# Performance work log

Hardware: AMD Instinct MI355X
Metric: run time of the kernel (lower is better)

Reference implementation:

```python
import jax, jax.numpy as jnp
import numpy as np

D, K, CIN, CD, COUT = 3, 16, 128, 32, 256
C = CIN + CD                  # 160 = C_in + C_delta after concat
DM = -(-COUT // C)            # depth_multiplier = ceil(C_out / C) = 2
N, I = 4, 2048                # batch, points per cloud; M = N*I = 8192


def _bn(x, g, b, eps=1e-5):
    # BatchNorm1d in training mode: biased batch statistics over dim 0
    mu = x.mean(0)
    v = x.var(0)
    return (x - mu) * jax.lax.rsqrt(v + eps) * g + b


def _knn(p, k):
    # knn_graph over ALL M points (wrapper passes no batch vector), loop=True
    d2 = jnp.sum(p * p, axis=1)
    dist = d2[:, None] + d2[None, :] - 2.0 * (p @ p.T)   # [M,M]
    _, idx = jax.lax.top_k(-dist, k)                     # [M,K], self first
    return idx


def _gconv(t, w, b, M):
    # grouped Conv1d(K, K*K, kernel=K, groups=K): t [M,K,K], w [K(cin), K(out/grp), K(tap)]
    return jnp.einsum('mcl,col->mco', t, w).reshape(M, K * K) + b


def _xconv(xf, pf, idx, w1a, b1a, g1a, be1a, w1b, b1b, g1b, be1b,
           w2, b2, g2a, be2a, wc2a, bc2a, g2b, be2b, wc2b, bc2b, g2c, be2c,
           wcd, bcd, wl, bl):
    M = pf.shape[0]
    rel = pf[idx] - pf[:, None, :]                       # [M,K,D] relative neighbor coords
    # mlp1: lift relative coords to C_delta features
    h = rel.reshape(M * K, D)
    h = _bn(jax.nn.elu(h @ w1a + b1a), g1a, be1a)
    h = _bn(jax.nn.elu(h @ w1b + b1b), g1b, be1b)
    x_star = jnp.concatenate([h.reshape(M, K, CD), xf[idx]], axis=-1)  # [M,K,C]
    x_star = x_star.transpose(0, 2, 1)                   # [M,C,K]
    # mlp2: learn KxK X-transformation from the K*D relative coords
    t = _bn(jax.nn.elu(rel.reshape(M, K * D) @ w2 + b2), g2a, be2a).reshape(M, K, K)
    t = _bn(jax.nn.elu(_gconv(t, wc2a, bc2a, M)), g2b, be2b).reshape(M, K, K)
    t = _bn(_gconv(t, wc2b, bc2b, M), g2c, be2c).reshape(M, K, K)
    xt = jnp.einsum('mck,mkj->mcj', x_star, t)           # [M,C,K] batched matmul
    # depthwise Conv1d(C, C*DM, K, groups=C) collapses K, then final Linear
    y = jnp.einsum('mcl,col->mco', xt, wcd).reshape(M, C * DM) + bcd
    return y @ wl + bl                                   # [M,COUT]


def setup_inputs() -> dict:
    key = jax.random.key(0)
    ks = jax.random.split(key, 16)
    r = lambda k, s: jax.random.normal(k, s, jnp.float32) * 0.1
    return dict(
        x=jax.random.normal(ks[0], (N, I, CIN), jnp.float32),
        pos=jax.random.normal(ks[1], (N, I, D), jnp.float32),
        w1a=r(ks[2], (D, CD)), b1a=r(ks[3], (CD,)), g1a=jnp.ones((CD,)), be1a=jnp.zeros((CD,)),
        w1b=r(ks[4], (CD, CD)), b1b=r(ks[5], (CD,)), g1b=jnp.ones((CD,)), be1b=jnp.zeros((CD,)),
        w2=r(ks[6], (D * K, K * K)), b2=r(ks[7], (K * K,)), g2a=jnp.ones((K * K,)), be2a=jnp.zeros((K * K,)),
        wc2a=r(ks[8], (K, K, K)), bc2a=r(ks[9], (K * K,)), g2b=jnp.ones((K * K,)), be2b=jnp.zeros((K * K,)),
        wc2b=r(ks[10], (K, K, K)), bc2b=r(ks[11], (K * K,)), g2c=jnp.ones((K * K,)), be2c=jnp.zeros((K * K,)),
        wcd=r(ks[12], (C, DM, K)), bcd=r(ks[13], (C * DM,)),
        wl=r(ks[14], (C * DM, COUT)), bl=r(ks[15], (COUT,)),
    )


def reference(x, pos, w1a, b1a, g1a, be1a, w1b, b1b, g1b, be1b,
              w2, b2, g2a, be2a, wc2a, bc2a, g2b, be2b, wc2b, bc2b, g2c, be2c,
              wcd, bcd, wl, bl):
    pf = pos.reshape(N * I, D)
    xf = x.reshape(N * I, CIN)
    idx = _knn(pf, K)
    out = _xconv(xf, pf, idx, w1a, b1a, g1a, be1a, w1b, b1b, g1b, be1b,
                 w2, b2, g2a, be2a, wc2a, bc2a, g2b, be2b, wc2b, bc2b, g2c, be2c,
                 wcd, bcd, wl, bl)
    return out.reshape(N, I, COUT)
```

## Files before the change

### kernel.cpp

```cpp
#include <hip/hip_runtime.h>
#include <math.h>

#define M_PTS 8192
#define MK    131072

typedef __attribute__((ext_vector_type(8))) short bf16x8;
typedef __attribute__((ext_vector_type(4))) float f32x4;
typedef __fp16 half2v __attribute__((ext_vector_type(2)));
union H2U { half2v h; unsigned u; };

__device__ __forceinline__ float elu(float v){ return v > 0.f ? v : __expf(v)-1.0f; }

__device__ __forceinline__ unsigned cvt_pk_bf16(float lo, float hi){
  unsigned r;
  asm("v_cvt_pk_bf16_f32 %0, %1, %2" : "=v"(r) : "v"(lo), "v"(hi));
  return r;
}
__device__ __forceinline__ unsigned short f2bf(float v){
  unsigned u = __float_as_uint(v);
  return (unsigned short)((u + 0x7FFFu + ((u>>16)&1u)) >> 16);
}
__device__ __forceinline__ unsigned pk_min_u16(unsigned a, unsigned b){
  unsigned r; asm("v_pk_min_u16 %0, %1, %2" : "=v"(r) : "v"(a), "v"(b)); return r;
}
__device__ __forceinline__ unsigned pk_max_u16(unsigned a, unsigned b){
  unsigned r; asm("v_pk_max_u16 %0, %1, %2" : "=v"(r) : "v"(a), "v"(b)); return r;
}

__device__ __forceinline__ unsigned distkey(float4 c, float qx, float qy, float qz, float d2q){
  #pragma clang fp contract(off)
  float dot  = __builtin_fmaf(c.z, qz, __builtin_fmaf(c.y, qy, __builtin_fmaf(c.x, qx, 0.0f)));
  float A    = d2q + c.w;
  float B    = 2.0f * dot;
  float dist = A - B;
  unsigned u = __float_as_uint(dist);
  return u ^ ((unsigned)((int)u >> 31) | 0x80000000u);
}

__global__ __launch_bounds__(512) void knn_kernel(const float* __restrict__ pos,
                                                  int* __restrict__ nidx,
                                                  float* __restrict__ st,
                                                  float4* __restrict__ pos4){
  __shared__ float4 cand[1024];
  __shared__ unsigned long long hits[8][64];
  int tid  = threadIdx.x;
  int lane = tid & 63;
  int wv   = tid >> 6;
  int q    = blockIdx.x*8 + wv;
  if (blockIdx.x == 0){
    for (int i = tid; i < 2048; i += 512) st[i] = 0.f;
  }
  float qx = pos[3*q], qy = pos[3*q+1], qz = pos[3*q+2];
  float d2q;
  {
    #pragma clang fp contract(off)
    d2q = (qx*qx + qy*qy) + qz*qz;
  }

  unsigned ka[8];
  #pragma unroll
  for (int s=0;s<8;s++) ka[s] = 0xFFFFFFFFu;

  for (int base = 0; base < M_PTS; base += 1024){
    for (int t = tid; t < 1024; t += 512){
      #pragma clang fp contract(off)
      int j = base + t;
      float x = pos[3*j], y = pos[3*j+1], z = pos[3*j+2];
      float d2v = (x*x + y*y) + z*z;
      float4 c = make_float4(x,y,z,d2v);
      cand[t] = c;
      if (pos4 && blockIdx.x == (base >> 10)) pos4[j] = c;
    }
    __syncthreads();
    #pragma unroll
    for (int k=0; k<8; k++){
      float4 c0 = cand[lane + k*128];
      float4 c1 = cand[lane + 64 + k*128];
      float dotA = c0.x*qx + c0.y*qy + c0.z*qz;
      float dotB = c1.x*qx + c1.y*qy + c1.z*qz;
      float dA = fmaxf((d2q + c0.w) - 2.0f*dotA, 0.f);
      float dB = fmaxf((d2q + c1.w) - 2.0f*dotB, 0.f);
      H2U pu; pu.h = __builtin_amdgcn_cvt_pkrtz(dA, dB);
      unsigned v = pu.u;
      #pragma unroll
      for (int s=0;s<8;s++){
        unsigned mn = pk_min_u16(v, ka[s]);
        unsigned mx = pk_max_u16(v, ka[s]);
        ka[s] = mn; v = mx;
      }
    }
    __syncthreads();
  }

  unsigned lo[8], hi[8];
  #pragma unroll
  for (int s=0;s<8;s++){ lo[s] = ka[s] & 0xFFFFu; hi[s] = ka[s] >> 16; }
  unsigned t16 = 0xFFFFu;
  for (int r=0; r<16; r++){
    unsigned head = min(lo[0], hi[0]);
    unsigned best = head;
    #pragma unroll
    for (int off=32; off>0; off>>=1){
      unsigned o = __shfl_xor(best, off, 64);
      best = min(best, o);
    }
    bool adv = (head == best);
    bool fromLo = lo[0] <= hi[0];
    bool aL = adv && fromLo;
    bool aH = adv && !fromLo;
    #pragma unroll
    for (int s=0;s<7;s++){
      lo[s] = aL ? lo[s+1] : lo[s];
      hi[s] = aH ? hi[s+1] : hi[s];
    }
    lo[7] = aL ? 0xFFFFu : lo[7];
    hi[7] = aH ? 0xFFFFu : hi[7];
    t16 = best;
  }
  unsigned tu = min(t16 + 2u, 0x7C00u);
  float thrF;
  asm("v_cvt_f32_f16 %0, %1" : "=v"(thrF) : "v"(tu));

  int cnt = 0;
  for (int base = 0; base < M_PTS; base += 1024){
    for (int t = tid; t < 1024; t += 512){
      #pragma clang fp contract(off)
      int j = base + t;
      float x = pos[3*j], y = pos[3*j+1], z = pos[3*j+2];
      float d2v = (x*x + y*y) + z*z;
      cand[t] = make_float4(x,y,z,d2v);
    }
    __syncthreads();
    #pragma unroll
    for (int k=0; k<16; k++){
      int idx = lane + k*64;
      int j = base + idx;
      float4 c = cand[idx];
      float dot = c.x*qx + c.y*qy + c.z*qz;
      bool hit = ((d2q + c.w) - 2.0f*dot) <= thrF;
      unsigned long long m = __ballot(hit);
      if (m){
        unsigned u = distkey(c, qx, qy, qz, d2q);
        if (hit){
          int slot = cnt + __popcll(m & ((1ull<<lane)-1ull));
          if (slot < 64) hits[wv][slot] = ((unsigned long long)u << 32) | (unsigned)j;
        }
        cnt += (int)__popcll(m);
      }
    }
    __syncthreads();
  }

  int cc = min(cnt, 64);
  unsigned long long mine = (lane < cc) ? hits[wv][lane] : ~0ull;
  for (int r=0; r<16; r++){
    unsigned long long best = mine;
    #pragma unroll
    for (int off=32; off>0; off>>=1){
      unsigned long long o = __shfl_xor(best, off, 64);
      best = (o < best) ? o : best;
    }
    if (mine == best) mine = ~0ull;
    if (lane == 0) nidx[q*16 + r] = (int)(unsigned)best;
  }
}

__global__ __launch_bounds__(256) void stats_a_kernel(const float* __restrict__ pos,
    const float4* __restrict__ pos4,
    const int* __restrict__ nidx,
    const float* __restrict__ w1a, const float* __restrict__ b1a,
    const float* __restrict__ w2,  const float* __restrict__ b2,
    const float* __restrict__ wl,  unsigned short* __restrict__ wlbf,
    float* __restrict__ tact,
    float* __restrict__ s1, float* __restrict__ s3){
  int tid = threadIdx.x;
  if (blockIdx.x < 512){
    __shared__ float relS[256][3];
    __shared__ float red[8][64];
    int r = blockIdx.x*256 + tid;
    int m = r >> 4;
    int j = nidx[r];
    if (pos4){
      float4 pj = pos4[j], pm = pos4[m];
      relS[tid][0] = pj.x-pm.x; relS[tid][1] = pj.y-pm.y; relS[tid][2] = pj.z-pm.z;
    } else {
      relS[tid][0] = pos[3*j  ]-pos[3*m  ];
      relS[tid][1] = pos[3*j+1]-pos[3*m+1];
      relS[tid][2] = pos[3*j+2]-pos[3*m+2];
    }
    __syncthreads();
    int c = tid & 31, g = tid >> 5;
    float w0=w1a[c], w1v=w1a[32+c], w2v=w1a[64+c], b=b1a[c];
    float s=0.f, q=0.f;
    for (int rr=g*32; rr<g*32+32; rr++){
      float h = elu(b + relS[rr][0]*w0 + relS[rr][1]*w1v + relS[rr][2]*w2v);
      s += h; q += h*h;
    }
    red[g][c]=s; red[g][32+c]=q;
    __syncthreads();
    if (tid < 64){
      float a=0.f;
      #pragma unroll
      for (int gg=0;gg<8;gg++) a += red[gg][tid];
      atomicAdd(&s1[tid], a);
    }
  } else if (blockIdx.x < 1536){
    __shared__ float relf[8][48];
    int m0 = (blockIdx.x-512)*8;
    if (pos4){
      for (int f = tid; f < 8*16; f += 256){
        int p = f >> 4, k = f & 15;
        int j = nidx[(m0+p)*16 + k];
        float4 pj = pos4[j], pm = pos4[m0+p];
        relf[p][k*3+0] = pj.x-pm.x;
        relf[p][k*3+1] = pj.y-pm.y;
        relf[p][k*3+2] = pj.z-pm.z;
      }
    } else {
      for (int f = tid; f < 8*48; f += 256){
        int p = f/48, kd = f%48, k = kd/3, d = kd%3;
        int j = nidx[(m0+p)*16 + k];
        relf[p][kd] = pos[3*j+d] - pos[3*(m0+p)+d];
      }
    }
    __syncthreads();
    float acc[8];
    #pragma unroll
    for (int p=0;p<8;p++) acc[p] = b2[tid];
    for (int kk=0; kk<48; kk++){
      float w = w2[kk*256 + tid];
      #pragma unroll
      for (int p=0;p<8;p++) acc[p] += relf[p][kk]*w;
    }
    float s=0.f, q=0.f;
    #pragma unroll
    for (int p=0;p<8;p++){
      float v = elu(acc[p]);
      s += v; q += v*v;
      tact[(size_t)(m0+p)*256 + tid] = v;
    }
    atomicAdd(&s3[tid], s); atomicAdd(&s3[256+tid], q);
  } else {
    int t = (blockIdx.x - 1536)*256 + tid;
    int lane = t & 63;
    int fr   = t >> 6;
    int k0   = (fr >> 4)*32 + (lane >> 4)*8;
    int col  = (fr & 15)*16 + (lane & 15);
    const float* wp = wl + (size_t)k0*256 + col;
    uint4 v;
    v.x = cvt_pk_bf16(wp[0],    wp[256]);
    v.y = cvt_pk_bf16(wp[512],  wp[768]);
    v.z = cvt_pk_bf16(wp[1024], wp[1280]);
    v.w = cvt_pk_bf16(wp[1536], wp[1792]);
    ((uint4*)wlbf)[t] = v;
  }
}

__global__ __launch_bounds__(256) void stats_b_kernel(const float* __restrict__ pos,
    const float4* __restrict__ pos4,
    const int* __restrict__ nidx,
    const float* __restrict__ w1a, const float* __restrict__ b1a,
    const float* __restrict__ s1,  const float* __restrict__ g1a, const float* __restrict__ be1a,
    const float* __restrict__ w1b, const float* __restrict__ b1b,
    float* __restrict__ tact,
    const float* __restrict__ s3,  const float* __restrict__ g2a, const float* __restrict__ be2a,
    const float* __restrict__ wc2a,const float* __restrict__ bc2a,
    unsigned short* __restrict__ h2c,
    float* __restrict__ s2, float* __restrict__ s4){
  int tid = threadIdx.x;
  const float invMK = 1.f/(float)MK;
  const float invM  = 1.f/8192.f;
  if (blockIdx.x < 1024){
    __shared__ float xnS[128][33];
    __shared__ float red[8][64];
    __shared__ float muA[32], ivA[32];
    if (tid < 32){
      float mu  = s1[tid]*invMK;
      float var = s1[32+tid]*invMK - mu*mu;
      muA[tid] = mu; ivA[tid] = rsqrtf(var+1e-5f)*g1a[tid];
    }
    __syncthreads();
    {
      int rl = tid >> 1;
      int r  = blockIdx.x*128 + rl;
      int m = r >> 4;
      int j = nidx[r];
      float rx, ry, rz;
      if (pos4){
        float4 pj = pos4[j], pm = pos4[m];
        rx = pj.x-pm.x; ry = pj.y-pm.y; rz = pj.z-pm.z;
      } else {
        rx = pos[3*j]-pos[3*m]; ry = pos[3*j+1]-pos[3*m+1]; rz = pos[3*j+2]-pos[3*m+2];
      }
      int c0 = (tid & 1)*16;
      #pragma unroll
      for (int u=0; u<16; u++){
        int cc = c0 + u;
        float h = elu(b1a[cc] + rx*w1a[cc] + ry*w1a[32+cc] + rz*w1a[64+cc]);
        xnS[rl][cc] = (h-muA[cc])*ivA[cc] + be1a[cc];
      }
    }
    __syncthreads();
    int o = tid & 31, g = tid >> 5;
    float wcol[32];
    #pragma unroll
    for (int cc=0;cc<32;cc++) wcol[cc] = w1b[cc*32+o];
    float bo = b1b[o], s=0.f, q=0.f;
    for (int rr=g*16; rr<g*16+16; rr++){
      float a = bo;
      #pragma unroll
      for (int cc=0;cc<32;cc++) a += xnS[rr][cc]*wcol[cc];
      float v = elu(a);
      s += v; q += v*v;
      if (h2c) h2c[(size_t)(blockIdx.x*128 + rr)*32 + o] = f2bf(v);
    }
    red[g][o]=s; red[g][32+o]=q;
    __syncthreads();
    if (tid < 64){
      float a=0.f;
      #pragma unroll
      for (int gg=0;gg<8;gg++) a += red[gg][tid];
      atomicAdd(&s2[tid], a);
    }
  } else {
    __shared__ float tn[8][256];
    int m0 = (blockIdx.x-1024)*8;
    float mu3  = s3[tid]*invM;
    float var3 = s3[256+tid]*invM - mu3*mu3;
    float i3   = rsqrtf(var3+1e-5f)*g2a[tid];
    float bb3  = be2a[tid];
    float tv[8];
    #pragma unroll
    for (int p=0;p<8;p++) tv[p] = tact[(size_t)(m0+p)*256 + tid];
    #pragma unroll
    for (int p=0;p<8;p++) tn[p][tid] = (tv[p]-mu3)*i3 + bb3;
    __syncthreads();
    int c = tid >> 4;
    float wreg[16];
    const float4* wv4 = (const float4*)(wc2a + tid*16);
    #pragma unroll
    for (int v=0; v<4; v++){ float4 f = wv4[v]; wreg[4*v]=f.x; wreg[4*v+1]=f.y; wreg[4*v+2]=f.z; wreg[4*v+3]=f.w; }
    float bias = bc2a[tid];
    float s=0.f, q=0.f;
    #pragma unroll
    for (int p=0;p<8;p++){
      float a2 = bias;
      #pragma unroll
      for (int l=0;l<16;l++) a2 += tn[p][c*16+l]*wreg[l];
      float v = elu(a2);
      s += v; q += v*v;
      tv[p] = v;
    }
    #pragma unroll
    for (int p=0;p<8;p++) tact[(size_t)(m0+p)*256 + tid] = tv[p];
    atomicAdd(&s4[tid], s); atomicAdd(&s4[256+tid], q);
  }
}

__global__ __launch_bounds__(256) void t3_stats_kernel(
    float* __restrict__ tact,
    const float* __restrict__ s4, const float* __restrict__ g2b, const float* __restrict__ be2b,
    const float* __restrict__ wc2b, const float* __restrict__ bc2b, float* __restrict__ s5){
  __shared__ float tn2[8][256];
  int m0 = blockIdx.x*8, tid = threadIdx.x;
  const float invM = 1.f/8192.f;
  float mu4  = s4[tid]*invM;
  float var4 = s4[256+tid]*invM - mu4*mu4;
  float i4   = rsqrtf(var4+1e-5f)*g2b[tid];
  float bb4  = be2b[tid];
  float tv[8];
  #pragma unroll
  for (int p=0;p<8;p++) tv[p] = tact[(size_t)(m0+p)*256 + tid];
  #pragma unroll
  for (int p=0;p<8;p++) tn2[p][tid] = (tv[p]-mu4)*i4 + bb4;
  __syncthreads();
  int c = tid >> 4;
  float w2reg[16];
  { const float4* wv4 = (const float4*)(wc2b + tid*16);
    #pragma unroll
    for (int v=0; v<4; v++){ float4 f = wv4[v]; w2reg[4*v]=f.x; w2reg[4*v+1]=f.y; w2reg[4*v+2]=f.z; w2reg[4*v+3]=f.w; } }
  float bias2 = bc2b[tid];
  float s=0.f, q=0.f;
  #pragma unroll
  for (int p=0;p<8;p++){
    float a3 = bias2;
    #pragma unroll
    for (int l=0;l<16;l++) a3 += tn2[p][c*16+l]*w2reg[l];
    s += a3; q += a3*a3;
    tv[p] = a3;
  }
  #pragma unroll
  for (int p=0;p<8;p++) tact[(size_t)(m0+p)*256 + tid] = tv[p];
  atomicAdd(&s5[tid], s); atomicAdd(&s5[256+tid], q);
}

#define PFM 4
__global__ __launch_bounds__(256) void final_mfma_kernel(
    const float* __restrict__ x, const float* __restrict__ pos,
    const float4* __restrict__ pos4, const int* __restrict__ nidx,
    const float* __restrict__ w1a, const float* __restrict__ b1a,
    const float* __restrict__ g1a, const float* __restrict__ be1a,
    const float* __restrict__ w1b, const float* __restrict__ b1b,
    const float* __restrict__ g1b, const float* __restrict__ be1b,
    const float* __restrict__ g2c, const float* __restrict__ be2c,
    const float* __restrict__ wcd, const float* __restrict__ bcd,
    const unsigned short* __restrict__ wlbf, const float* __restrict__ bl,
    const unsigned short* __restrict__ h2c,
    const float* __restrict__ st,
    float* __restrict__ out){
  __shared__ float tA[PFM][256];
  __shared__ unsigned short xs[PFM*32*17];
  __shared__ unsigned short yh[16][328];
  __shared__ int   sidx[PFM*16];
  __shared__ float mu1[32], i1g[32], mu2[32], i2g[32];
  int tid = threadIdx.x;
  int m0  = blockIdx.x*PFM;
  const float invMK = 1.f/(float)MK;
  const float invM  = 1.f/8192.f;

  if (tid < PFM*16) sidx[tid] = nidx[m0*16 + tid];
  if (tid < 32){
    float mu  = st[tid]*invMK;
    float var = st[32+tid]*invMK - mu*mu;
    mu1[tid] = mu; i1g[tid] = rsqrtf(var+1e-5f)*g1a[tid];
    float mu_2  = st[64+tid]*invMK;
    float var_2 = st[96+tid]*invMK - mu_2*mu_2;
    mu2[tid] = mu_2; i2g[tid] = rsqrtf(var_2+1e-5f)*g1b[tid];
  }
  {
    unsigned short* yz = &yh[PFM][0];
    for (int i = tid; i < (16-PFM)*328; i += 256) yz[i] = 0;
  }
  {
    float mu5 = st[1152+tid]*invM, var5 = st[1408+tid]*invM - mu5*mu5;
    float i5 = rsqrtf(var5+1e-5f)*g2c[tid], bb5 = be2c[tid];
    #pragma unroll
    for (int p=0;p<PFM;p++){
      float v = out[(size_t)(m0+p)*256 + tid];
      tA[p][tid] = (v-mu5)*i5 + bb5;
    }
  }
  __syncthreads();

  {
    int row = tid >> 2;
    int p = row >> 4, k = row & 15;
    int q8 = (tid & 3)*8;
    if (h2c){
      size_t r = (size_t)blockIdx.x*64 + row;
      uint4 hv = *(const uint4*)(h2c + r*32 + q8);
      unsigned dw[4] = {hv.x, hv.y, hv.z, hv.w};
      #pragma unroll
      for (int d=0; d<4; ++d){
        int o0 = q8 + 2*d, o1 = o0 + 1;
        float v0 = __uint_as_float(dw[d] << 16);
        float v1 = __uint_as_float(dw[d] & 0xFFFF0000u);
        xs[(p*32 + o0)*17 + k] = f2bf((v0-mu2[o0])*i2g[o0] + be1b[o0]);
        xs[(p*32 + o1)*17 + k] = f2bf((v1-mu2[o1])*i2g[o1] + be1b[o1]);
      }
    } else {
      int m = m0 + p;
      int j = sidx[row];
      float rx, ry, rz;
      if (pos4){
        float4 pj = pos4[j], pm = pos4[m];
        rx = pj.x-pm.x; ry = pj.y-pm.y; rz = pj.z-pm.z;
      } else {
        rx = pos[3*j]-pos[3*m]; ry = pos[3*j+1]-pos[3*m+1]; rz = pos[3*j+2]-pos[3*m+2];
      }
      float xn[32];
      #pragma unroll
      for (int cc=0; cc<32; cc++){
        float h = elu(b1a[cc] + rx*w1a[cc] + ry*w1a[32+cc] + rz*w1a[64+cc]);
        xn[cc] = (h-mu1[cc])*i1g[cc] + be1a[cc];
      }
      #pragma unroll
      for (int oo=0; oo<8; oo++){
        int o = q8 + oo;
        float a = b1b[o];
        #pragma unroll
        for (int cc=0; cc<32; cc++) a += xn[cc]*w1b[cc*32+o];
        float h2v = elu(a);
        xs[(p*32 + o)*17 + k] = f2bf((h2v-mu2[o])*i2g[o] + be1b[o]);
      }
    }
  }
  __syncthreads();

  for (int pair = tid; pair < PFM*160; pair += 256){
    int p = pair / 160, cch = pair % 160;
    float av[16];
    if (cch < 32){
      #pragma unroll
      for (int k16=0;k16<16;k16++)
        av[k16] = __uint_as_float((unsigned)xs[(p*32+cch)*17 + k16] << 16);
    } else {
      #pragma unroll
      for (int k16=0;k16<16;k16++) av[k16] = x[(size_t)sidx[p*16+k16]*128 + (cch-32)];
    }
    float xt[16];
    #pragma unroll
    for (int j16=0;j16<16;j16++) xt[j16]=0.f;
    #pragma unroll
    for (int k16=0;k16<16;k16++){
      float a = av[k16];
      #pragma unroll
      for (int j16=0;j16<16;j16++) xt[j16] += a*tA[p][k16*16+j16];
    }
    float y0 = bcd[cch*2], y1 = bcd[cch*2+1];
    #pragma unroll
    for (int l=0;l<16;l++){
      y0 += xt[l]*wcd[cch*32 + l];
      y1 += xt[l]*wcd[cch*32 + 16 + l];
    }
    *(unsigned*)&yh[p][cch*2] = cvt_pk_bf16(y0, y1);
  }
  __syncthreads();

  {
    int lane = tid & 63;
    int wvi  = tid >> 6;
    int lrow = lane & 15;
    int lgrp = lane >> 4;
    const bf16x8* wb = (const bf16x8*)wlbf;
    f32x4 acc[4];
    #pragma unroll
    for (int nt=0; nt<4; ++nt) acc[nt] = (f32x4){0.f,0.f,0.f,0.f};
    #pragma unroll 1
    for (int kt = 0; kt < 10; ++kt){
      bf16x8 ah = *(const bf16x8*)&yh[lrow][kt*32 + lgrp*8];
      #pragma unroll
      for (int nt = 0; nt < 4; ++nt){
        bf16x8 bh = wb[(size_t)((kt*16 + wvi*4 + nt)*64) + lane];
        acc[nt] = __builtin_amdgcn_mfma_f32_16x16x32_bf16(ah, bh, acc[nt], 0, 0, 0);
      }
    }
    if (lgrp == 0){
      #pragma unroll
      for (int nt=0; nt<4; ++nt){
        int col = wvi*64 + nt*16 + lrow;
        float bv = bl[col];
        #pragma unroll
        for (int r=0;r<4;r++){
          int orow = r;
          out[(size_t)(m0+orow)*256 + col] = acc[nt][r] + bv;
        }
      }
    }
  }
}

#define PF 4
__global__ __launch_bounds__(256) void final_kernel(
    const float* __restrict__ x, const float* __restrict__ pos, const int* __restrict__ nidx,
    const float* __restrict__ w1a, const float* __restrict__ b1a,
    const float* __restrict__ g1a, const float* __restrict__ be1a,
    const float* __restrict__ w1b, const float* __restrict__ b1b,
    const float* __restrict__ g1b, const float* __restrict__ be1b,
    const float* __restrict__ g2c, const float* __restrict__ be2c,
    const float* __restrict__ wcd, const float* __restrict__ bcd,
    const float* __restrict__ wl,  const float* __restrict__ bl,
    const float* __restrict__ st,
    float* __restrict__ out){
  __shared__ float tA[PF][256];
  __shared__ float xs[PF*32*17];
  __shared__ float yy[PF][320];
  __shared__ int   sidx[PF*16];
  __shared__ float mu1[32], i1g[32], mu2[32], i2g[32];
  int tid = threadIdx.x;
  int m0  = blockIdx.x*PF;
  const float invMK = 1.f/(float)MK;
  const float invM  = 1.f/8192.f;

  if (tid < PF*16) sidx[tid] = nidx[m0*16 + tid];
  if (tid < 32){
    float mu  = st[tid]*invMK;
    float var = st[32+tid]*invMK - mu*mu;
    mu1[tid] = mu; i1g[tid] = rsqrtf(var+1e-5f)*g1a[tid];
    float mu_2  = st[64+tid]*invMK;
    float var_2 = st[96+tid]*invMK - mu_2*mu_2;
    mu2[tid] = mu_2; i2g[tid] = rsqrtf(var_2+1e-5f)*g1b[tid];
  }
  {
    float mu5 = st[1152+tid]*invM, var5 = st[1408+tid]*invM - mu5*mu5;
    float i5 = rsqrtf(var5+1e-5f)*g2c[tid], bb5 = be2c[tid];
    #pragma unroll
    for (int p=0;p<PF;p++){
      float v = out[(size_t)(m0+p)*256 + tid];
      tA[p][tid] = (v-mu5)*i5 + bb5;
    }
  }
  __syncthreads();

  {
    int row = tid >> 2;
    int p = row >> 4, k = row & 15;
    int q8 = (tid & 3)*8;
    int m = m0 + p;
    int j = sidx[p*16 + k];
    float rx = pos[3*j]-pos[3*m], ry = pos[3*j+1]-pos[3*m+1], rz = pos[3*j+2]-pos[3*m+2];
    float xn[32];
    #pragma unroll
    for (int cc=0; cc<32; cc++){
      float h = elu(b1a[cc] + rx*w1a[cc] + ry*w1a[32+cc] + rz*w1a[64+cc]);
      xn[cc] = (h-mu1[cc])*i1g[cc] + be1a[cc];
    }
    #pragma unroll
    for (int oo=0; oo<8; oo++){
      int o = q8 + oo;
      float a = b1b[o];
      #pragma unroll
      for (int cc=0; cc<32; cc++) a += xn[cc]*w1b[cc*32+o];
      float h2v = elu(a);
      xs[(p*32 + o)*17 + k] = (h2v-mu2[o])*i2g[o] + be1b[o];
    }
  }
  __syncthreads();

  for (int pair = tid; pair < PF*160; pair += 256){
    int p = pair / 160, cch = pair % 160;
    float av[16];
    if (cch < 32){
      #pragma unroll
      for (int k16=0;k16<16;k16++) av[k16] = xs[(p*32+cch)*17 + k16];
    } else {
      #pragma unroll
      for (int k16=0;k16<16;k16++) av[k16] = x[(size_t)sidx[p*16+k16]*128 + (cch-32)];
    }
    float xt[16];
    #pragma unroll
    for (int j16=0;j16<16;j16++) xt[j16]=0.f;
    #pragma unroll
    for (int k16=0;k16<16;k16++){
      float a = av[k16];
      #pragma unroll
      for (int j16=0;j16<16;j16++) xt[j16] += a*tA[p][k16*16+j16];
    }
    float y0 = bcd[cch*2], y1 = bcd[cch*2+1];
    #pragma unroll
    for (int l=0;l<16;l++){
      y0 += xt[l]*wcd[cch*32 + l];
      y1 += xt[l]*wcd[cch*32 + 16 + l];
    }
    yy[p][cch*2] = y0; yy[p][cch*2+1] = y1;
  }
  __syncthreads();

  float accO[PF];
  #pragma unroll
  for (int p=0;p<PF;p++) accO[p] = bl[tid];
  for (int q=0;q<320;q++){
    float w = wl[q*256 + tid];
    #pragma unroll
    for (int p=0;p<PF;p++) accO[p] += yy[p][q]*w;
  }
  #pragma unroll
  for (int p=0;p<PF;p++) out[(size_t)(m0+p)*256 + tid] = accO[p];
}

extern "C" void kernel_launch(void* const* d_in, const int* in_sizes, int n_in,
                              void* d_out, int out_size, void* d_ws, size_t ws_size,
                              hipStream_t stream){
  const float* x    = (const float*)d_in[0];
  const float* pos  = (const float*)d_in[1];
  const float* w1a  = (const float*)d_in[2];
  const float* b1a  = (const float*)d_in[3];
  const float* g1a  = (const float*)d_in[4];
  const float* be1a = (const float*)d_in[5];
  const float* w1b  = (const float*)d_in[6];
  const float* b1b  = (const float*)d_in[7];
  const float* g1b  = (const float*)d_in[8];
  const float* be1b = (const float*)d_in[9];
  const float* w2   = (const float*)d_in[10];
  const float* b2   = (const float*)d_in[11];
  const float* g2a  = (const float*)d_in[12];
  const float* be2a = (const float*)d_in[13];
  const float* wc2a = (const float*)d_in[14];
  const float* bc2a = (const float*)d_in[15];
  const float* g2b  = (const float*)d_in[16];
  const float* be2b = (const float*)d_in[17];
  const float* wc2b = (const float*)d_in[18];
  const float* bc2b = (const float*)d_in[19];
  const float* g2c  = (const float*)d_in[20];
  const float* be2c = (const float*)d_in[21];
  const float* wcd  = (const float*)d_in[22];
  const float* bcd  = (const float*)d_in[23];
  const float* wl   = (const float*)d_in[24];
  const float* bl   = (const float*)d_in[25];
  float* out = (float*)d_out;

  char* ws = (char*)d_ws;
  int*   nidx = (int*)(ws + 0);
  float* st   = (float*)(ws + 524288);
  float* s1 = st;
  float* s2 = st + 64;
  float* s3 = st + 128;
  float* s4 = st + 640;
  float* s5 = st + 1152;
  bool big  = ws_size >= (size_t)696320;
  bool big2 = ws_size >= (size_t)824320;
  bool big3 = ws_size >= (size_t)9212928;
  unsigned short* wlbf = big  ? (unsigned short*)(ws + 532480) : (unsigned short*)0;
  float4*         pos4 = big2 ? (float4*)(ws + 696320)         : (float4*)0;
  unsigned short* h2c  = big3 ? (unsigned short*)(ws + 824320) : (unsigned short*)0;

  knn_kernel<<<1024,512,0,stream>>>(pos, nidx, st, pos4);
  stats_a_kernel<<<(big ? 1576 : 1536),256,0,stream>>>(pos, pos4, nidx, w1a, b1a, w2, b2,
                                                       wl, wlbf, out, s1, s3);
  stats_b_kernel<<<2048,256,0,stream>>>(pos, pos4, nidx, w1a, b1a, s1, g1a, be1a, w1b, b1b,
                                        out, s3, g2a, be2a, wc2a, bc2a, h2c, s2, s4);
  t3_stats_kernel<<<1024,256,0,stream>>>(out, s4, g2b, be2b, wc2b, bc2b, s5);
  if (big){
    final_mfma_kernel<<<2048,256,0,stream>>>(x, pos, pos4, nidx,
                                             w1a, b1a, g1a, be1a, w1b, b1b, g1b, be1b,
                                             g2c, be2c, wcd, bcd, wlbf, bl, h2c, st, out);
  } else {
    final_kernel<<<2048,256,0,stream>>>(x, pos, nidx,
                                        w1a, b1a, g1a, be1a, w1b, b1b, g1b, be1b,
                                        g2c, be2c, wcd, bcd, wl, bl, st, out);
  }
}
```

Measured before the change: 328.9 us.

## Fuse kNN search with first-layer stats and wl bf16 conversion

Adds a fused kernel that runs the kNN top-16 search, computes the mlp1 first-layer and mlp2 first-layer ELU activations and their batch statistics for the block's queries, and uses extra blocks to convert wl to bf16. This removes the separate stats_a launch and its re-gather of neighbor positions. Stats zeroing moves to a hipMemsetAsync. The extra per-block epilogue uses LDS atomics and raises LDS use, which may lower kNN occupancy. The fallback path now passes null h2c pointers.

```diff
diff --git a/kernel.cpp b/kernel.cpp
--- a/kernel.cpp
+++ b/kernel.cpp
@@ -35,6 +35,210 @@
   float dist = A - B;
   unsigned u = __float_as_uint(dist);
   return u ^ ((unsigned)((int)u >> 31) | 0x80000000u);
+}
+
+__global__ __launch_bounds__(512) void knn_fused_kernel(const float* __restrict__ pos,
+    int* __restrict__ nidx, float* __restrict__ st, float4* __restrict__ pos4,
+    const float* __restrict__ w1a, const float* __restrict__ b1a,
+    const float* __restrict__ w2,  const float* __restrict__ b2,
+    const float* __restrict__ wl,  unsigned short* __restrict__ wlbf,
+    float* __restrict__ tact,
+    float* __restrict__ s1, float* __restrict__ s3){
+  int tid  = threadIdx.x;
+  if (blockIdx.x >= 1024){
+    int t = (blockIdx.x - 1024)*512 + tid;
+    int lane = t & 63;
+    int fr   = t >> 6;
+    int k0   = (fr >> 4)*32 + (lane >> 4)*8;
+    int col  = (fr & 15)*16 + (lane & 15);
+    const float* wp = wl + (size_t)k0*256 + col;
+    uint4 v;
+    v.x = cvt_pk_bf16(wp[0],    wp[256]);
+    v.y = cvt_pk_bf16(wp[512],  wp[768]);
+    v.z = cvt_pk_bf16(wp[1024], wp[1280]);
+    v.w = cvt_pk_bf16(wp[1536], wp[1792]);
+    ((uint4*)wlbf)[t] = v;
+    return;
+  }
+  __shared__ float4 cand[1024];
+  __shared__ unsigned long long hits[8][64];
+  __shared__ int   sidxS[8][16];
+  __shared__ float relf[8][48];
+  __shared__ float sAcc[64];
+  __shared__ float s3L[512];
+  int lane = tid & 63;
+  int wv   = tid >> 6;
+  int q    = blockIdx.x*8 + wv;
+  if (tid < 64) sAcc[tid] = 0.f;
+  float qx = pos[3*q], qy = pos[3*q+1], qz = pos[3*q+2];
+  float d2q;
+  {
+    #pragma clang fp contract(off)
+    d2q = (qx*qx + qy*qy) + qz*qz;
+  }
+
+  unsigned ka[8];
+  #pragma unroll
+  for (int s=0;s<8;s++) ka[s] = 0xFFFFFFFFu;
+
+  for (int base = 0; base < M_PTS; base += 1024){
+    for (int t = tid; t < 1024; t += 512){
+      #pragma clang fp contract(off)
+      int j = base + t;
+      float x = pos[3*j], y = pos[3*j+1], z = pos[3*j+2];
+      float d2v = (x*x + y*y) + z*z;
+      float4 c = make_float4(x,y,z,d2v);
+      cand[t] = c;
+      if (blockIdx.x == (base >> 10)) pos4[j] = c;
+    }
+    __syncthreads();
+    #pragma unroll
+    for (int k=0; k<8; k++){
+      float4 c0 = cand[lane + k*128];
+      float4 c1 = cand[lane + 64 + k*128];
+      float dotA = c0.x*qx + c0.y*qy + c0.z*qz;
+      float dotB = c1.x*qx + c1.y*qy + c1.z*qz;
+      float dA = fmaxf((d2q + c0.w) - 2.0f*dotA, 0.f);
+      float dB = fmaxf((d2q + c1.w) - 2.0f*dotB, 0.f);
+      H2U pu; pu.h = __builtin_amdgcn_cvt_pkrtz(dA, dB);
+      unsigned v = pu.u;
+      #pragma unroll
+      for (int s=0;s<8;s++){
+        unsigned mn = pk_min_u16(v, ka[s]);
+        unsigned mx = pk_max_u16(v, ka[s]);
+        ka[s] = mn; v = mx;
+      }
+    }
+    __syncthreads();
+  }
+
+  unsigned lo[8], hi[8];
+  #pragma unroll
+  for (int s=0;s<8;s++){ lo[s] = ka[s] & 0xFFFFu; hi[s] = ka[s] >> 16; }
+  unsigned t16 = 0xFFFFu;
+  for (int r=0; r<16; r++){
+    unsigned head = min(lo[0], hi[0]);
+    unsigned best = head;
+    #pragma unroll
+    for (int off=32; off>0; off>>=1){
+      unsigned o = __shfl_xor(best, off, 64);
+      best = min(best, o);
+    }
+    bool adv = (head == best);
+    bool fromLo = lo[0] <= hi[0];
+    bool aL = adv && fromLo;
+    bool aH = adv && !fromLo;
+    #pragma unroll
+    for (int s=0;s<7;s++){
+      lo[s] = aL ? lo[s+1] : lo[s];
+      hi[s] = aH ? hi[s+1] : hi[s];
+    }
+    lo[7] = aL ? 0xFFFFu : lo[7];
+    hi[7] = aH ? 0xFFFFu : hi[7];
+    t16 = best;
+  }
+  unsigned tu = min(t16 + 2u, 0x7C00u);
+  float thrF;
+  asm("v_cvt_f32_f16 %0, %1" : "=v"(thrF) : "v"(tu));
+
+  int cnt = 0;
+  for (int base = 0; base < M_PTS; base += 1024){
+    for (int t = tid; t < 1024; t += 512){
+      #pragma clang fp contract(off)
+      int j = base + t;
+      float x = pos[3*j], y = pos[3*j+1], z = pos[3*j+2];
+      float d2v = (x*x + y*y) + z*z;
+      cand[t] = make_float4(x,y,z,d2v);
+    }
+    __syncthreads();
+    #pragma unroll
+    for (int k=0; k<16; k++){
+      int idx = lane + k*64;
+      int j = base + idx;
+      float4 c = cand[idx];
+      float dot = c.x*qx + c.y*qy + c.z*qz;
+      bool hit = ((d2q + c.w) - 2.0f*dot) <= thrF;
+      unsigned long long m = __ballot(hit);
+      if (m){
+        unsigned u = distkey(c, qx, qy, qz, d2q);
+        if (hit){
+          int slot = cnt + __popcll(m & ((1ull<<lane)-1ull));
+          if (slot < 64) hits[wv][slot] = ((unsigned long long)u << 32) | (unsigned)j;
+        }
+        cnt += (int)__popcll(m);
+      }
+    }
+    __syncthreads();
+  }
+
+  int cc = min(cnt, 64);
+  unsigned long long mine = (lane < cc) ? hits[wv][lane] : ~0ull;
+  for (int r=0; r<16; r++){
+    unsigned long long best = mine;
+    #pragma unroll
+    for (int off=32; off>0; off>>=1){
+      unsigned long long o = __shfl_xor(best, off, 64);
+      best = (o < best) ? o : best;
+    }
+    if (mine == best) mine = ~0ull;
+    if (lane == 0){
+      int bi = (int)(unsigned)best;
+      nidx[q*16 + r] = bi;
+      sidxS[wv][r]   = bi;
+    }
+  }
+  __syncthreads();
+
+  {
+    int row = tid >> 2;
+    int c0  = (tid & 3) * 8;
+    int p = row >> 4, k = row & 15;
+    int j = sidxS[p][k];
+    int m = blockIdx.x*8 + p;
+    float rx = pos[3*j]-pos[3*m], ry = pos[3*j+1]-pos[3*m+1], rz = pos[3*j+2]-pos[3*m+2];
+    #pragma unroll
+    for (int u=0; u<8; u++){
+      int cch = c0 + u;
+      float h = elu(b1a[cch] + rx*w1a[cch] + ry*w1a[32+cch] + rz*w1a[64+cch]);
+      atomicAdd(&sAcc[cch], h);
+      atomicAdd(&sAcc[32+cch], h*h);
+    }
+  }
+  if (tid < 128){
+    int p = tid >> 4, k = tid & 15;
+    int j = sidxS[p][k];
+    int m = blockIdx.x*8 + p;
+    #pragma unroll
+    for (int d=0; d<3; d++) relf[p][k*3+d] = pos[3*j+d] - pos[3*m+d];
+  }
+  __syncthreads();
+  float sT = 0.f, qT = 0.f;
+  int   chT = tid & 255;
+  {
+    int pp = (tid >> 8) * 4;
+    float acc[4];
+    #pragma unroll
+    for (int pi=0; pi<4; pi++) acc[pi] = b2[chT];
+    for (int kk=0; kk<48; kk++){
+      float w = w2[kk*256 + chT];
+      #pragma unroll
+      for (int pi=0; pi<4; pi++) acc[pi] += relf[pp+pi][kk]*w;
+    }
+    int m0 = blockIdx.x*8;
+    #pragma unroll
+    for (int pi=0; pi<4; pi++){
+      float v = elu(acc[pi]);
+      sT += v; qT += v*v;
+      tact[(size_t)(m0+pp+pi)*256 + chT] = v;
+    }
+    if (tid < 256){ s3L[chT] = sT; s3L[256+chT] = qT; }
+  }
+  __syncthreads();
+  if (tid < 64) atomicAdd(&s1[tid], sAcc[tid]);
+  if (tid >= 256){
+    atomicAdd(&s3[chT],     s3L[chT]     + sT);
+    atomicAdd(&s3[256+chT], s3L[256+chT] + qT);
+  }
 }
 
 __global__ __launch_bounds__(512) void knn_kernel(const float* __restrict__ pos,
@@ -704,19 +908,31 @@
   float4*         pos4 = big2 ? (float4*)(ws + 696320)         : (float4*)0;
   unsigned short* h2c  = big3 ? (unsigned short*)(ws + 824320) : (unsigned short*)0;
 
-  knn_kernel<<<1024,512,0,stream>>>(pos, nidx, st, pos4);
-  stats_a_kernel<<<(big ? 1576 : 1536),256,0,stream>>>(pos, pos4, nidx, w1a, b1a, w2, b2,
-                                                       wl, wlbf, out, s1, s3);
-  stats_b_kernel<<<2048,256,0,stream>>>(pos, pos4, nidx, w1a, b1a, s1, g1a, be1a, w1b, b1b,
-                                        out, s3, g2a, be2a, wc2a, bc2a, h2c, s2, s4);
-  t3_stats_kernel<<<1024,256,0,stream>>>(out, s4, g2b, be2b, wc2b, bc2b, s5);
-  if (big){
+  if (big3){
+    hipMemsetAsync(st, 0, 8192, stream);
+    knn_fused_kernel<<<1044,512,0,stream>>>(pos, nidx, st, pos4,
+                                            w1a, b1a, w2, b2, wl, wlbf, out, s1, s3);
+    stats_b_kernel<<<2048,256,0,stream>>>(pos, pos4, nidx, w1a, b1a, s1, g1a, be1a, w1b, b1b,
+                                          out, s3, g2a, be2a, wc2a, bc2a, h2c, s2, s4);
+    t3_stats_kernel<<<1024,256,0,stream>>>(out, s4, g2b, be2b, wc2b, bc2b, s5);
     final_mfma_kernel<<<2048,256,0,stream>>>(x, pos, pos4, nidx,
                                              w1a, b1a, g1a, be1a, w1b, b1b, g1b, be1b,
                                              g2c, be2c, wcd, bcd, wlbf, bl, h2c, st, out);
   } else {
-    final_kernel<<<2048,256,0,stream>>>(x, pos, nidx,
-                                        w1a, b1a, g1a, be1a, w1b, b1b, g1b, be1b,
-                                        g2c, be2c, wcd, bcd, wl, bl, st, out);
-  }
-}
+    knn_kernel<<<1024,512,0,stream>>>(pos, nidx, st, pos4);
+    stats_a_kernel<<<(big ? 1576 : 1536),256,0,stream>>>(pos, pos4, nidx, w1a, b1a, w2, b2,
+                                                         wl, wlbf, out, s1, s3);
+    stats_b_kernel<<<2048,256,0,stream>>>(pos, pos4, nidx, w1a, b1a, s1, g1a, be1a, w1b, b1b,
+                                          out, s3, g2a, be2a, wc2a, bc2a, (unsigned short*)0, s2, s4);
+    t3_stats_kernel<<<1024,256,0,stream>>>(out, s4, g2b, be2b, wc2b, bc2b, s5);
+    if (big){
+      final_mfma_kernel<<<2048,256,0,stream>>>(x, pos, pos4, nidx,
+                                               w1a, b1a, g1a, be1a, w1b, b1b, g1b, be1b,
+                                               g2c, be2c, wcd, bcd, wlbf, bl, (unsigned short*)0, st, out);
+    } else {
+      final_kernel<<<2048,256,0,stream>>>(x, pos, nidx,
+                                          w1a, b1a, g1a, be1a, w1b, b1b, g1b, be1b,
+                                          g2c, be2c, wcd, bcd, wl, bl, st, out);
+    }
+  }
+}
```

New measurement: 352.1 us. 1.07x slower.
